# Kernel optimization log

Measured on AMD Instinct MI355X. Metric: run time of the kernel, lower is better.

The kernel has to match this reference:

```python
import jax, jax.numpy as jnp
import numpy as np

B, S, D = 4, 2048, 1024
H, HD = 16, 64
MLP = 4 * D
EPS = 1e-6


def _rms_norm(x, scale):
    var = jnp.mean(jnp.square(x), axis=-1, keepdims=True)
    return x * jax.lax.rsqrt(var + EPS) * scale


def setup_inputs() -> dict:
    key = jax.random.key(0)
    ks = jax.random.split(key, 8)
    sd = D ** -0.5
    return {
        "x": jax.random.normal(ks[0], (B, S, D), jnp.float32),
        "pre_norm_scale": jnp.ones((D,), jnp.float32),
        "w_mlp_in": jax.random.normal(ks[1], (D, MLP), jnp.float32) * sd,   # MLPBlockInput, no bias
        "wq": jax.random.normal(ks[2], (D, H, HD), jnp.float32) * sd,
        "wk": jax.random.normal(ks[3], (D, H, HD), jnp.float32) * sd,
        "wv": jax.random.normal(ks[4], (D, H, HD), jnp.float32) * sd,
        "w_mlp_out": jax.random.normal(ks[5], (MLP, D), jnp.float32) * (MLP ** -0.5),
        "b_mlp_out": jnp.zeros((D,), jnp.float32),
        "w_attn_out": jax.random.normal(ks[6], (H, HD, D), jnp.float32) * sd,  # DenseGeneral axis=(-2,-1)
        "b_attn_out": jnp.zeros((D,), jnp.float32),
    }


def reference(x, pre_norm_scale, w_mlp_in, wq, wk, wv, w_mlp_out, b_mlp_out,
              w_attn_out, b_attn_out):
    residual = x
    xn = _rms_norm(x, pre_norm_scale)                      # pre_norm (TPNorm)

    # QKVMLPDense: fused MLP-input + QKV projections
    h = jax.nn.gelu(jnp.einsum("bsd,df->bsf", xn, w_mlp_in))   # [B,S,MLP]
    q = jnp.einsum("bsd,dhk->bshk", xn, wq)                    # [B,S,H,HD]
    k = jnp.einsum("bsd,dhk->bshk", xn, wk)
    v = jnp.einsum("bsd,dhk->bshk", xn, wv)

    # dot_product_attention (mask=None)
    scores = jnp.einsum("bqhd,bkhd->bhqk", q, k) / jnp.sqrt(jnp.asarray(HD, x.dtype))
    probs = jax.nn.softmax(scores, axis=-1)
    attn_v = jnp.einsum("bhqk,bkhd->bqhd", probs, v)           # [B,S,H,HD]

    # AttnMLPOut: mlp_out + attn_out
    mlp_out = jnp.einsum("bsf,fd->bsd", h, w_mlp_out) + b_mlp_out
    attn_out = jnp.einsum("bqhk,hkd->bqd", attn_v, w_attn_out) + b_attn_out
    block_out = mlp_out + attn_out                              # dropout is identity (train=False)
    return residual + block_out
```

## Files before the change

### kernel.cpp

```cpp
#include <hip/hip_runtime.h>
#include <cstdint>
#include <cstddef>

typedef float floatx4 __attribute__((ext_vector_type(4)));
typedef short bf16x8 __attribute__((ext_vector_type(8)));

#define MFMA(a, b, c) __builtin_amdgcn_mfma_f32_16x16x32_bf16((a), (b), (c), 0, 0, 0)

__device__ __forceinline__ unsigned short f2bf(float f) {
  union { float f; unsigned int u; } v; v.f = f;
  unsigned int u = v.u;
  unsigned int r = (u + 0x7FFFu + ((u >> 16) & 1u)) >> 16;
  return (unsigned short)r;
}

__device__ __forceinline__ void gload_lds16(const unsigned short* g, unsigned short* s) {
  __builtin_amdgcn_global_load_lds(
      (const __attribute__((address_space(1))) unsigned int*)g,
      (__attribute__((address_space(3))) unsigned int*)s, 16, 0, 0);
}

__global__ __launch_bounds__(256) void prep_all(
    const float* __restrict__ w_mlp_in, const float* __restrict__ wq,
    const float* __restrict__ wk, const float* __restrict__ wv,
    const float* __restrict__ w_mlp_out, const float* __restrict__ w_attn_out,
    const float* __restrict__ x, const float* __restrict__ pns,
    unsigned short* __restrict__ wcatT, unsigned short* __restrict__ wcat2T,
    unsigned short* __restrict__ xn) {
  __shared__ float tile[32][33];
  __shared__ float ws4[4];
  int id = blockIdx.x;
  if (id >= 12288) {
    int row = id - 12288;
    const float4 v = ((const float4*)(x + (size_t)row * 1024))[threadIdx.x];
    float ss = v.x * v.x + v.y * v.y + v.z * v.z + v.w * v.w;
#pragma unroll
    for (int off = 1; off < 64; off <<= 1) ss += __shfl_xor(ss, off, 64);
    if ((threadIdx.x & 63) == 0) ws4[threadIdx.x >> 6] = ss;
    __syncthreads();
    float tot = ws4[0] + ws4[1] + ws4[2] + ws4[3];
    float rs = rsqrtf(tot * (1.0f / 1024.0f) + 1e-6f);
    const float4 sc = ((const float4*)pns)[threadIdx.x];
    uint2 o;
    o.x = (unsigned)f2bf(v.x * rs * sc.x) | ((unsigned)f2bf(v.y * rs * sc.y) << 16);
    o.y = (unsigned)f2bf(v.z * rs * sc.z) | ((unsigned)f2bf(v.w * rs * sc.w) << 16);
    ((uint2*)(xn + (size_t)row * 1024))[threadIdx.x] = o;
    return;
  }
  const float* src; unsigned short* dst; int C, ldd, bx, by, q;
  if (id < 4096)       { src = w_mlp_in;   dst = wcatT;                        C = 4096; ldd = 1024; q = id;         bx = q & 127; by = q >> 7; }
  else if (id < 5120)  { src = wq;         dst = wcatT + (size_t)4096 * 1024;  C = 1024; ldd = 1024; q = id - 4096;  bx = q & 31;  by = q >> 5; }
  else if (id < 6144)  { src = wk;         dst = wcatT + (size_t)5120 * 1024;  C = 1024; ldd = 1024; q = id - 5120;  bx = q & 31;  by = q >> 5; }
  else if (id < 7168)  { src = wv;         dst = wcatT + (size_t)6144 * 1024;  C = 1024; ldd = 1024; q = id - 6144;  bx = q & 31;  by = q >> 5; }
  else if (id < 11264) { src = w_mlp_out;  dst = wcat2T;                       C = 1024; ldd = 5120; q = id - 7168;  bx = q & 31;  by = q >> 5; }
  else                 { src = w_attn_out; dst = wcat2T + 4096;                C = 1024; ldd = 5120; q = id - 11264; bx = q & 31;  by = q >> 5; }
  int tx = threadIdx.x & 31, ty = threadIdx.x >> 5;
#pragma unroll
  for (int i = 0; i < 4; i++) {
    int r = ty + i * 8;
    tile[r][tx] = src[(size_t)(by * 32 + r) * C + bx * 32 + tx];
  }
  __syncthreads();
#pragma unroll
  for (int i = 0; i < 4; i++) {
    int r = ty + i * 8;
    dst[(size_t)(bx * 32 + r) * ldd + by * 32 + tx] = f2bf(tile[tx][r]);
  }
}

template <int MODE>
__global__ __launch_bounds__(256, 2) void gemm_bt(
    const unsigned short* __restrict__ A, const unsigned short* __restrict__ BT,
    int K, void* __restrict__ outp,
    const float* __restrict__ bias1, const float* __restrict__ bias2,
    const float* __restrict__ resid,
    int msplit, int tm, int tn,
    unsigned short* __restrict__ q_out, unsigned short* __restrict__ k_out,
    unsigned short* __restrict__ v_out) {
  __shared__ unsigned short As[2][128 * 32];
  __shared__ unsigned short Bs[2][128 * 32];

  int id = blockIdx.x + gridDim.x * blockIdx.y;
  int xcd = id & 7, j = id >> 3;
  int mh = xcd % msplit, nq = xcd / msplit;
  int by = mh * tm + j / tn;
  int bx = nq * tn + j % tn;
  int m0 = by * 128, n0 = bx * 128;

  int t = threadIdx.x, lane = t & 63, wave = t >> 6;
  int l15 = lane & 15, quad = lane >> 4;
  int wm = (wave & 1) * 64, wn = (wave >> 1) * 64;

  floatx4 acc[4][4] = {};

  int lr = lane >> 2;
  int lg = (lane & 3) ^ ((lane >> 3) & 3);
  int ch0 = wave * 2, ch1 = wave * 2 + 1;
  const unsigned short* gA0 = A + (size_t)(m0 + ch0 * 16 + lr) * K + lg * 8;
  const unsigned short* gA1 = A + (size_t)(m0 + ch1 * 16 + lr) * K + lg * 8;
  const unsigned short* gB0 = BT + (size_t)(n0 + ch0 * 16 + lr) * K + lg * 8;
  const unsigned short* gB1 = BT + (size_t)(n0 + ch1 * 16 + lr) * K + lg * 8;
  unsigned short* sA0[2] = {&As[0][ch0 * 512 + lane * 8], &As[1][ch0 * 512 + lane * 8]};
  unsigned short* sA1[2] = {&As[0][ch1 * 512 + lane * 8], &As[1][ch1 * 512 + lane * 8]};
  unsigned short* sB0[2] = {&Bs[0][ch0 * 512 + lane * 8], &Bs[1][ch0 * 512 + lane * 8]};
  unsigned short* sB1[2] = {&Bs[0][ch1 * 512 + lane * 8], &Bs[1][ch1 * 512 + lane * 8]};

  int fo = (4 * l15 + (quad ^ ((l15 >> 1) & 3))) * 8;
  int ca = (wm >> 4);
  int cb = (wn >> 4);

  for (int kt = 0; kt < K; kt += 64) {
    __syncthreads();
#pragma unroll
    for (int kk = 0; kk < 2; kk++) {
      int kg = kt + kk * 32;
      gload_lds16(gA0 + kg, sA0[kk]);
      gload_lds16(gA1 + kg, sA1[kk]);
      gload_lds16(gB0 + kg, sB0[kk]);
      gload_lds16(gB1 + kg, sB1[kk]);
    }
    __syncthreads();
#pragma unroll
    for (int kk = 0; kk < 2; kk++) {
      bf16x8 a[4], b[4];
#pragma unroll
      for (int im = 0; im < 4; im++)
        a[im] = *(const bf16x8*)&As[kk][(ca + im) * 512 + fo];
#pragma unroll
      for (int in_ = 0; in_ < 4; in_++)
        b[in_] = *(const bf16x8*)&Bs[kk][(cb + in_) * 512 + fo];
#pragma unroll
      for (int im = 0; im < 4; im++)
#pragma unroll
        for (int in_ = 0; in_ < 4; in_++)
          acc[im][in_] = MFMA(a[im], b[in_], acc[im][in_]);
    }
  }

#pragma unroll
  for (int im = 0; im < 4; im++) {
#pragma unroll
    for (int in_ = 0; in_ < 4; in_++) {
#pragma unroll
      for (int r = 0; r < 4; r++) {
        int row = m0 + wm + im * 16 + quad * 4 + r;
        int col = n0 + wn + in_ * 16 + l15;
        float v = acc[im][in_][r];
        if constexpr (MODE == 6) {
          if (n0 < 4096) {
            float z = 0.7978845608028654f * (v + 0.044715f * v * v * v);
            float e = __expf(2.0f * z);
            float th = 1.0f - 2.0f / (e + 1.0f);
            ((unsigned short*)outp)[(size_t)row * 5120 + col] = f2bf(0.5f * v * (1.0f + th));
          } else {
            int seg = (n0 - 4096) >> 10;
            int cs = col - 4096 - (seg << 10);
            int b_ = row >> 11, s = row & 2047, h = cs >> 6, hd = cs & 63;
            if (seg == 0)
              q_out[(((size_t)(b_ * 16 + h)) * 2048 + s) * 64 + hd] = f2bf(v * 0.125f);
            else if (seg == 1)
              k_out[(((size_t)(b_ * 16 + h)) * 2048 + s) * 64 + hd] = f2bf(v);
            else
              v_out[(((size_t)(b_ * 16 + h)) * 64 + hd) * 2048 + s] = f2bf(v);
          }
        } else {
          size_t idx = (size_t)row * 1024 + col;
          ((float*)outp)[idx] = v + bias1[col] + bias2[col] + resid[idx];
        }
      }
    }
  }
}

__global__ __launch_bounds__(256, 2) void flash_attn(
    const unsigned short* __restrict__ q_buf, const unsigned short* __restrict__ k_buf,
    const unsigned short* __restrict__ v_buf, unsigned short* __restrict__ cat) {
  constexpr int S = 2048, HD = 64;
  constexpr int LK = 72, LV = 72, LP = 68;
  __shared__ unsigned short Ks[2][64 * LK];
  __shared__ unsigned short Vs[2][64 * LV];
  __shared__ unsigned short Ps[4][32 * LP];

  int id = blockIdx.x + gridDim.x * blockIdx.y;
  int xcd = id & 7, j = id >> 3;
  int bh = xcd * 8 + (j >> 4);
  int qbk = j & 15;

  int t = threadIdx.x, lane = t & 63, wave = t >> 6;
  int l15 = lane & 15, quad = lane >> 4;

  const unsigned short* qp = q_buf + (size_t)bh * S * HD;
  const unsigned short* kp = k_buf + (size_t)bh * S * HD;
  const unsigned short* vp = v_buf + (size_t)bh * HD * S;

  int q0 = qbk * 128 + wave * 32;
  bf16x8 aQ[2][2];
#pragma unroll
  for (int qf = 0; qf < 2; qf++) {
    aQ[qf][0] = *(const bf16x8*)&qp[(size_t)(q0 + qf * 16 + l15) * HD + quad * 8];
    aQ[qf][1] = *(const bf16x8*)&qp[(size_t)(q0 + qf * 16 + l15) * HD + 32 + quad * 8];
  }

  floatx4 acc_o[2][4] = {};
  float lrow[2][4] = {};

  int kr = t >> 3, kc = (t & 7) * 8;

  uint4 rK0 = *(const uint4*)&kp[(size_t)kr * HD + kc];
  uint4 rK1 = *(const uint4*)&kp[(size_t)(kr + 32) * HD + kc];
  uint4 rV0 = *(const uint4*)&vp[(size_t)kr * S + kc];
  uint4 rV1 = *(const uint4*)&vp[(size_t)(kr + 32) * S + kc];
  *(uint4*)&Ks[0][kr * LK + kc] = rK0;
  *(uint4*)&Ks[0][(kr + 32) * LK + kc] = rK1;
  *(uint4*)&Vs[0][kr * LV + kc] = rV0;
  *(uint4*)&Vs[0][(kr + 32) * LV + kc] = rV1;
  rK0 = *(const uint4*)&kp[(size_t)(64 + kr) * HD + kc];
  rK1 = *(const uint4*)&kp[(size_t)(64 + kr + 32) * HD + kc];
  rV0 = *(const uint4*)&vp[(size_t)kr * S + 64 + kc];
  rV1 = *(const uint4*)&vp[(size_t)(kr + 32) * S + 64 + kc];
  asm volatile("s_waitcnt lgkmcnt(0)" ::: "memory");
  __syncthreads();

  for (int kv = 0; kv < S; kv += 64) {
    int cur = (kv >> 6) & 1;
    if (kv + 64 < S) {
      *(uint4*)&Ks[cur ^ 1][kr * LK + kc] = rK0;
      *(uint4*)&Ks[cur ^ 1][(kr + 32) * LK + kc] = rK1;
      *(uint4*)&Vs[cur ^ 1][kr * LV + kc] = rV0;
      *(uint4*)&Vs[cur ^ 1][(kr + 32) * LV + kc] = rV1;
    }

    floatx4 z[2][4];
#pragma unroll
    for (int cg = 0; cg < 4; cg++) {
      bf16x8 bk0 = *(const bf16x8*)&Ks[cur][(cg * 16 + l15) * LK + quad * 8];
      bf16x8 bk1 = *(const bf16x8*)&Ks[cur][(cg * 16 + l15) * LK + 32 + quad * 8];
#pragma unroll
      for (int qf = 0; qf < 2; qf++) {
        floatx4 acc = {};
        acc = MFMA(aQ[qf][0], bk0, acc);
        acc = MFMA(aQ[qf][1], bk1, acc);
        z[qf][cg] = acc;
      }
    }
    if (kv + 128 < S) {
      rK0 = *(const uint4*)&kp[(size_t)(kv + 128 + kr) * HD + kc];
      rK1 = *(const uint4*)&kp[(size_t)(kv + 128 + kr + 32) * HD + kc];
      rV0 = *(const uint4*)&vp[(size_t)kr * S + kv + 128 + kc];
      rV1 = *(const uint4*)&vp[(size_t)(kr + 32) * S + kv + 128 + kc];
    }
#pragma unroll
    for (int qf = 0; qf < 2; qf++)
#pragma unroll
      for (int cg = 0; cg < 4; cg++)
#pragma unroll
        for (int r = 0; r < 4; r++) {
          float e = __expf(z[qf][cg][r]);
          lrow[qf][r] += e;
          Ps[wave][(qf * 16 + quad * 4 + r) * LP + cg * 16 + l15] = f2bf(e);
        }
    asm volatile("s_waitcnt lgkmcnt(0)" ::: "memory");
#pragma unroll
    for (int c = 0; c < 2; c++) {
      bf16x8 aP[2];
#pragma unroll
      for (int qf = 0; qf < 2; qf++) {
        const unsigned short* pp = &Ps[wave][(qf * 16 + l15) * LP + c * 32 + quad * 8];
        ((uint2*)&aP[qf])[0] = *(const uint2*)pp;
        ((uint2*)&aP[qf])[1] = *(const uint2*)(pp + 4);
      }
#pragma unroll
      for (int n = 0; n < 4; n++) {
        bf16x8 bv = *(const bf16x8*)&Vs[cur][(n * 16 + l15) * LV + c * 32 + quad * 8];
        acc_o[0][n] = MFMA(aP[0], bv, acc_o[0][n]);
        acc_o[1][n] = MFMA(aP[1], bv, acc_o[1][n]);
      }
    }
    __syncthreads();
  }

#pragma unroll
  for (int qf = 0; qf < 2; qf++)
#pragma unroll
    for (int r = 0; r < 4; r++) {
      float s = lrow[qf][r];
#pragma unroll
      for (int off = 1; off < 16; off <<= 1) s += __shfl_xor(s, off, 16);
      lrow[qf][r] = s;
    }

  int b_ = bh >> 4, h = bh & 15;
#pragma unroll
  for (int qf = 0; qf < 2; qf++)
#pragma unroll
    for (int r = 0; r < 4; r++) {
      float inv = 1.0f / lrow[qf][r];
      int srow = q0 + qf * 16 + quad * 4 + r;
      size_t base = ((size_t)(b_ * 2048 + srow)) * 5120 + 4096 + h * 64;
#pragma unroll
      for (int n = 0; n < 4; n++)
        cat[base + n * 16 + l15] = f2bf(acc_o[qf][n][r] * inv);
    }
}

extern "C" void kernel_launch(void* const* d_in, const int* in_sizes, int n_in,
                              void* d_out, int out_size, void* d_ws, size_t ws_size,
                              hipStream_t stream) {
  (void)in_sizes; (void)n_in; (void)out_size; (void)ws_size;
  const float* x          = (const float*)d_in[0];
  const float* pns        = (const float*)d_in[1];
  const float* w_mlp_in   = (const float*)d_in[2];
  const float* wq         = (const float*)d_in[3];
  const float* wk         = (const float*)d_in[4];
  const float* wv         = (const float*)d_in[5];
  const float* w_mlp_out  = (const float*)d_in[6];
  const float* b_mlp_out  = (const float*)d_in[7];
  const float* w_attn_out = (const float*)d_in[8];
  const float* b_attn_out = (const float*)d_in[9];
  float* out = (float*)d_out;

  char* ws = (char*)d_ws;
  size_t off = 0;
  auto alloc = [&](size_t bytes) {
    void* p = ws + off;
    off += (bytes + 255) & ~(size_t)255;
    return p;
  };
  const size_t M = 8192;
  unsigned short* xn     = (unsigned short*)alloc(M * 1024 * 2);
  unsigned short* wcatT  = (unsigned short*)alloc((size_t)7168 * 1024 * 2);
  unsigned short* wcat2T = (unsigned short*)alloc((size_t)1024 * 5120 * 2);
  unsigned short* cat    = (unsigned short*)alloc(M * 5120 * 2);
  unsigned short* qb     = (unsigned short*)alloc(M * 1024 * 2);
  unsigned short* kb     = (unsigned short*)alloc(M * 1024 * 2);
  unsigned short* vb     = (unsigned short*)alloc(M * 1024 * 2);

  prep_all<<<dim3(20480), 256, 0, stream>>>(
      w_mlp_in, wq, wk, wv, w_mlp_out, w_attn_out, x, pns, wcatT, wcat2T, xn);

  gemm_bt<6><<<dim3(56, 64), 256, 0, stream>>>(
      xn, wcatT, 1024, cat, nullptr, nullptr, nullptr, 2, 32, 14, qb, kb, vb);

  flash_attn<<<dim3(16, 64), 256, 0, stream>>>(qb, kb, vb, cat);

  gemm_bt<7><<<dim3(8, 64), 256, 0, stream>>>(
      cat, wcat2T, 5120, out, b_mlp_out, b_attn_out, x, 2, 32, 2, nullptr, nullptr, nullptr);
}
```

Before: 549.7 us.

## Use packed bf16 conversion, nontemporal epilogue stores, and raise flash-attn occupancy

```diff
diff --git a/kernel.cpp b/kernel.cpp
--- a/kernel.cpp
+++ b/kernel.cpp
@@ -14,10 +14,23 @@
   return (unsigned short)r;
 }
 
+__device__ __forceinline__ unsigned int f2bf2(float lo, float hi) {
+  unsigned int r;
+  asm("v_cvt_pk_bf16_f32 %0, %1, %2" : "=v"(r) : "v"(lo), "v"(hi));
+  return r;
+}
+
 __device__ __forceinline__ void gload_lds16(const unsigned short* g, unsigned short* s) {
   __builtin_amdgcn_global_load_lds(
       (const __attribute__((address_space(1))) unsigned int*)g,
       (__attribute__((address_space(3))) unsigned int*)s, 16, 0, 0);
+}
+
+__device__ __forceinline__ float gelu_f(float v) {
+  float z = 0.7978845608028654f * (v + 0.044715f * v * v * v);
+  float e = __expf(2.0f * z);
+  float th = 1.0f - 2.0f / (e + 1.0f);
+  return 0.5f * v * (1.0f + th);
 }
 
 __global__ __launch_bounds__(256) void prep_all(
@@ -42,8 +55,8 @@
     float rs = rsqrtf(tot * (1.0f / 1024.0f) + 1e-6f);
     const float4 sc = ((const float4*)pns)[threadIdx.x];
     uint2 o;
-    o.x = (unsigned)f2bf(v.x * rs * sc.x) | ((unsigned)f2bf(v.y * rs * sc.y) << 16);
-    o.y = (unsigned)f2bf(v.z * rs * sc.z) | ((unsigned)f2bf(v.w * rs * sc.w) << 16);
+    o.x = f2bf2(v.x * rs * sc.x, v.y * rs * sc.y);
+    o.y = f2bf2(v.z * rs * sc.z, v.w * rs * sc.w);
     ((uint2*)(xn + (size_t)row * 1024))[threadIdx.x] = o;
     return;
   }
@@ -141,42 +154,60 @@
   for (int im = 0; im < 4; im++) {
 #pragma unroll
     for (int in_ = 0; in_ < 4; in_++) {
-#pragma unroll
-      for (int r = 0; r < 4; r++) {
-        int row = m0 + wm + im * 16 + quad * 4 + r;
-        int col = n0 + wn + in_ * 16 + l15;
-        float v = acc[im][in_][r];
-        if constexpr (MODE == 6) {
-          if (n0 < 4096) {
-            float z = 0.7978845608028654f * (v + 0.044715f * v * v * v);
-            float e = __expf(2.0f * z);
-            float th = 1.0f - 2.0f / (e + 1.0f);
-            ((unsigned short*)outp)[(size_t)row * 5120 + col] = f2bf(0.5f * v * (1.0f + th));
-          } else {
-            int seg = (n0 - 4096) >> 10;
-            int cs = col - 4096 - (seg << 10);
-            int b_ = row >> 11, s = row & 2047, h = cs >> 6, hd = cs & 63;
-            if (seg == 0)
-              q_out[(((size_t)(b_ * 16 + h)) * 2048 + s) * 64 + hd] = f2bf(v * 0.125f);
-            else if (seg == 1)
-              k_out[(((size_t)(b_ * 16 + h)) * 2048 + s) * 64 + hd] = f2bf(v);
-            else
-              v_out[(((size_t)(b_ * 16 + h)) * 64 + hd) * 2048 + s] = f2bf(v);
+      int row0 = m0 + wm + im * 16 + quad * 4;
+      int col = n0 + wn + in_ * 16 + l15;
+      if constexpr (MODE == 6) {
+        if (n0 < 4096) {
+#pragma unroll
+          for (int r = 0; r < 4; r += 2) {
+            unsigned u = f2bf2(gelu_f(acc[im][in_][r]), gelu_f(acc[im][in_][r + 1]));
+            __builtin_nontemporal_store((unsigned short)u,
+                &((unsigned short*)outp)[(size_t)(row0 + r) * 5120 + col]);
+            __builtin_nontemporal_store((unsigned short)(u >> 16),
+                &((unsigned short*)outp)[(size_t)(row0 + r + 1) * 5120 + col]);
           }
         } else {
-          size_t idx = (size_t)row * 1024 + col;
-          ((float*)outp)[idx] = v + bias1[col] + bias2[col] + resid[idx];
+          int seg = (n0 - 4096) >> 10;
+          int cs = col - 4096 - (seg << 10);
+          int h = cs >> 6, hd = cs & 63;
+          int b_ = row0 >> 11, s0 = row0 & 2047;
+          if (seg == 2) {
+            unsigned long long o =
+                (unsigned long long)f2bf2(acc[im][in_][0], acc[im][in_][1]) |
+                ((unsigned long long)f2bf2(acc[im][in_][2], acc[im][in_][3]) << 32);
+            __builtin_nontemporal_store(o,
+                (unsigned long long*)&v_out[(((size_t)(b_ * 16 + h)) * 64 + hd) * 2048 + s0]);
+          } else {
+            float sc = (seg == 0) ? 0.125f : 1.0f;
+            unsigned short* dst = (seg == 0) ? q_out : k_out;
+#pragma unroll
+            for (int r = 0; r < 4; r += 2) {
+              unsigned u = f2bf2(acc[im][in_][r] * sc, acc[im][in_][r + 1] * sc);
+              __builtin_nontemporal_store((unsigned short)u,
+                  &dst[(((size_t)(b_ * 16 + h)) * 2048 + s0 + r) * 64 + hd]);
+              __builtin_nontemporal_store((unsigned short)(u >> 16),
+                  &dst[(((size_t)(b_ * 16 + h)) * 2048 + s0 + r + 1) * 64 + hd]);
+            }
+          }
         }
-      }
-    }
-  }
-}
-
-__global__ __launch_bounds__(256, 2) void flash_attn(
+      } else {
+        float bsum = bias1[col] + bias2[col];
+#pragma unroll
+        for (int r = 0; r < 4; r++) {
+          size_t idx = (size_t)(row0 + r) * 1024 + col;
+          float res = __builtin_nontemporal_load(&resid[idx]);
+          __builtin_nontemporal_store(acc[im][in_][r] + bsum + res, &((float*)outp)[idx]);
+        }
+      }
+    }
+  }
+}
+
+__global__ __launch_bounds__(256, 3) void flash_attn(
     const unsigned short* __restrict__ q_buf, const unsigned short* __restrict__ k_buf,
     const unsigned short* __restrict__ v_buf, unsigned short* __restrict__ cat) {
   constexpr int S = 2048, HD = 64;
-  constexpr int LK = 72, LV = 72, LP = 68;
+  constexpr int LK = 68, LV = 68, LP = 68;
   __shared__ unsigned short Ks[2][64 * LK];
   __shared__ unsigned short Vs[2][64 * LV];
   __shared__ unsigned short Ps[4][32 * LP];
@@ -252,13 +283,20 @@
 #pragma unroll
     for (int qf = 0; qf < 2; qf++)
 #pragma unroll
-      for (int cg = 0; cg < 4; cg++)
-#pragma unroll
-        for (int r = 0; r < 4; r++) {
-          float e = __expf(z[qf][cg][r]);
-          lrow[qf][r] += e;
-          Ps[wave][(qf * 16 + quad * 4 + r) * LP + cg * 16 + l15] = f2bf(e);
-        }
+      for (int cg = 0; cg < 4; cg++) {
+        float e0 = __expf(z[qf][cg][0]);
+        float e1 = __expf(z[qf][cg][1]);
+        float e2 = __expf(z[qf][cg][2]);
+        float e3 = __expf(z[qf][cg][3]);
+        lrow[qf][0] += e0; lrow[qf][1] += e1;
+        lrow[qf][2] += e2; lrow[qf][3] += e3;
+        unsigned p01 = f2bf2(e0, e1), p23 = f2bf2(e2, e3);
+        unsigned short* base = &Ps[wave][(qf * 16 + quad * 4) * LP + cg * 16 + l15];
+        base[0 * LP] = (unsigned short)p01;
+        base[1 * LP] = (unsigned short)(p01 >> 16);
+        base[2 * LP] = (unsigned short)p23;
+        base[3 * LP] = (unsigned short)(p23 >> 16);
+      }
     asm volatile("s_waitcnt lgkmcnt(0)" ::: "memory");
 #pragma unroll
     for (int c = 0; c < 2; c++) {
@@ -297,9 +335,12 @@
       float inv = 1.0f / lrow[qf][r];
       int srow = q0 + qf * 16 + quad * 4 + r;
       size_t base = ((size_t)(b_ * 2048 + srow)) * 5120 + 4096 + h * 64;
-#pragma unroll
-      for (int n = 0; n < 4; n++)
-        cat[base + n * 16 + l15] = f2bf(acc_o[qf][n][r] * inv);
+      unsigned u01 = f2bf2(acc_o[qf][0][r] * inv, acc_o[qf][1][r] * inv);
+      unsigned u23 = f2bf2(acc_o[qf][2][r] * inv, acc_o[qf][3][r] * inv);
+      __builtin_nontemporal_store((unsigned short)u01,        &cat[base + 0 * 16 + l15]);
+      __builtin_nontemporal_store((unsigned short)(u01 >> 16), &cat[base + 1 * 16 + l15]);
+      __builtin_nontemporal_store((unsigned short)u23,        &cat[base + 2 * 16 + l15]);
+      __builtin_nontemporal_store((unsigned short)(u23 >> 16), &cat[base + 3 * 16 + l15]);
     }
 }
 
```

After: 542.0 us. About the same (-1.4%).

## Use nontemporal stores, pack V epilogue writes, retune flash-attn occupancy and LDS padding

Applied to the files above, without the earlier changes.

```diff
diff --git a/kernel.cpp b/kernel.cpp
--- a/kernel.cpp
+++ b/kernel.cpp
@@ -18,6 +18,13 @@
   __builtin_amdgcn_global_load_lds(
       (const __attribute__((address_space(1))) unsigned int*)g,
       (__attribute__((address_space(3))) unsigned int*)s, 16, 0, 0);
+}
+
+__device__ __forceinline__ float gelu_f(float v) {
+  float z = 0.7978845608028654f * (v + 0.044715f * v * v * v);
+  float e = __expf(2.0f * z);
+  float th = 1.0f - 2.0f / (e + 1.0f);
+  return 0.5f * v * (1.0f + th);
 }
 
 __global__ __launch_bounds__(256) void prep_all(
@@ -141,42 +148,56 @@
   for (int im = 0; im < 4; im++) {
 #pragma unroll
     for (int in_ = 0; in_ < 4; in_++) {
-#pragma unroll
-      for (int r = 0; r < 4; r++) {
-        int row = m0 + wm + im * 16 + quad * 4 + r;
-        int col = n0 + wn + in_ * 16 + l15;
-        float v = acc[im][in_][r];
-        if constexpr (MODE == 6) {
-          if (n0 < 4096) {
-            float z = 0.7978845608028654f * (v + 0.044715f * v * v * v);
-            float e = __expf(2.0f * z);
-            float th = 1.0f - 2.0f / (e + 1.0f);
-            ((unsigned short*)outp)[(size_t)row * 5120 + col] = f2bf(0.5f * v * (1.0f + th));
-          } else {
-            int seg = (n0 - 4096) >> 10;
-            int cs = col - 4096 - (seg << 10);
-            int b_ = row >> 11, s = row & 2047, h = cs >> 6, hd = cs & 63;
-            if (seg == 0)
-              q_out[(((size_t)(b_ * 16 + h)) * 2048 + s) * 64 + hd] = f2bf(v * 0.125f);
-            else if (seg == 1)
-              k_out[(((size_t)(b_ * 16 + h)) * 2048 + s) * 64 + hd] = f2bf(v);
-            else
-              v_out[(((size_t)(b_ * 16 + h)) * 64 + hd) * 2048 + s] = f2bf(v);
+      int row0 = m0 + wm + im * 16 + quad * 4;
+      int col = n0 + wn + in_ * 16 + l15;
+      if constexpr (MODE == 6) {
+        if (n0 < 4096) {
+#pragma unroll
+          for (int r = 0; r < 4; r++) {
+            __builtin_nontemporal_store(f2bf(gelu_f(acc[im][in_][r])),
+                &((unsigned short*)outp)[(size_t)(row0 + r) * 5120 + col]);
           }
         } else {
-          size_t idx = (size_t)row * 1024 + col;
-          ((float*)outp)[idx] = v + bias1[col] + bias2[col] + resid[idx];
+          int seg = (n0 - 4096) >> 10;
+          int cs = col - 4096 - (seg << 10);
+          int h = cs >> 6, hd = cs & 63;
+          int b_ = row0 >> 11, s0 = row0 & 2047;
+          if (seg == 2) {
+            unsigned long long o =
+                (unsigned long long)((unsigned)f2bf(acc[im][in_][0]) |
+                                     ((unsigned)f2bf(acc[im][in_][1]) << 16)) |
+                ((unsigned long long)((unsigned)f2bf(acc[im][in_][2]) |
+                                      ((unsigned)f2bf(acc[im][in_][3]) << 16)) << 32);
+            __builtin_nontemporal_store(o,
+                (unsigned long long*)&v_out[(((size_t)(b_ * 16 + h)) * 64 + hd) * 2048 + s0]);
+          } else {
+            float sc = (seg == 0) ? 0.125f : 1.0f;
+            unsigned short* dst = (seg == 0) ? q_out : k_out;
+#pragma unroll
+            for (int r = 0; r < 4; r++) {
+              __builtin_nontemporal_store(f2bf(acc[im][in_][r] * sc),
+                  &dst[(((size_t)(b_ * 16 + h)) * 2048 + s0 + r) * 64 + hd]);
+            }
+          }
+        }
+      } else {
+        float bsum = bias1[col] + bias2[col];
+#pragma unroll
+        for (int r = 0; r < 4; r++) {
+          size_t idx = (size_t)(row0 + r) * 1024 + col;
+          float res = __builtin_nontemporal_load(&resid[idx]);
+          __builtin_nontemporal_store(acc[im][in_][r] + bsum + res, &((float*)outp)[idx]);
         }
       }
     }
   }
 }
 
-__global__ __launch_bounds__(256, 2) void flash_attn(
+__global__ __launch_bounds__(256, 3) void flash_attn(
     const unsigned short* __restrict__ q_buf, const unsigned short* __restrict__ k_buf,
     const unsigned short* __restrict__ v_buf, unsigned short* __restrict__ cat) {
   constexpr int S = 2048, HD = 64;
-  constexpr int LK = 72, LV = 72, LP = 68;
+  constexpr int LK = 68, LV = 68, LP = 68;
   __shared__ unsigned short Ks[2][64 * LK];
   __shared__ unsigned short Vs[2][64 * LV];
   __shared__ unsigned short Ps[4][32 * LP];
@@ -219,7 +240,8 @@
   rV0 = *(const uint4*)&vp[(size_t)kr * S + 64 + kc];
   rV1 = *(const uint4*)&vp[(size_t)(kr + 32) * S + 64 + kc];
   asm volatile("s_waitcnt lgkmcnt(0)" ::: "memory");
-  __syncthreads();
+  __builtin_amdgcn_s_barrier();
+  __builtin_amdgcn_sched_barrier(0);
 
   for (int kv = 0; kv < S; kv += 64) {
     int cur = (kv >> 6) & 1;
@@ -276,7 +298,9 @@
         acc_o[1][n] = MFMA(aP[1], bv, acc_o[1][n]);
       }
     }
-    __syncthreads();
+    asm volatile("s_waitcnt lgkmcnt(0)" ::: "memory");
+    __builtin_amdgcn_s_barrier();
+    __builtin_amdgcn_sched_barrier(0);
   }
 
 #pragma unroll
@@ -299,7 +323,8 @@
       size_t base = ((size_t)(b_ * 2048 + srow)) * 5120 + 4096 + h * 64;
 #pragma unroll
       for (int n = 0; n < 4; n++)
-        cat[base + n * 16 + l15] = f2bf(acc_o[qf][n][r] * inv);
+        __builtin_nontemporal_store(f2bf(acc_o[qf][n][r] * inv),
+                                    &cat[base + n * 16 + l15]);
     }
 }
 
```

Result: no change. 546.7 us (-0.5%).
